# Kernel tuning notes

Measured on AMD Instinct MI355X. Metric: run time of the kernel, lower is better.

## Reference

```python
import jax, jax.numpy as jnp
import numpy as np

HIDDEN = 2048
N_HEADS = 16
HEAD_DIM = HIDDEN // N_HEADS  # 128
KV_DIM = HEAD_DIM             # multi_query: 1 kv head
INTER = 4 * HIDDEN
EPS = 1e-5


def setup_inputs() -> dict:
    key = jax.random.key(0)
    ks = jax.random.split(key, 16)
    s = 0.02
    d = dict(
        hidden_states=jax.random.normal(ks[0], (4, 2048, HIDDEN), jnp.float32),
        ln1_g=jnp.ones((HIDDEN,), jnp.float32),
        ln1_b=jnp.zeros((HIDDEN,), jnp.float32),
        ln2_g=jnp.ones((HIDDEN,), jnp.float32),
        ln2_b=jnp.zeros((HIDDEN,), jnp.float32),
        wq=jax.random.normal(ks[1], (HIDDEN, HIDDEN), jnp.float32) * s,
        bq=jnp.zeros((HIDDEN,), jnp.float32),
        wkv=jax.random.normal(ks[2], (HIDDEN, 2 * KV_DIM), jnp.float32) * s,
        bkv=jnp.zeros((2 * KV_DIM,), jnp.float32),
        wo=jax.random.normal(ks[3], (HIDDEN, HIDDEN), jnp.float32) * s,
        bo=jnp.zeros((HIDDEN,), jnp.float32),
        wfc=jax.random.normal(ks[4], (HIDDEN, INTER), jnp.float32) * s,
        bfc=jnp.zeros((INTER,), jnp.float32),
        wproj=jax.random.normal(ks[5], (INTER, HIDDEN), jnp.float32) * s,
        bproj=jnp.zeros((HIDDEN,), jnp.float32),
    )
    return d


def _ln(x, g, b):
    m = jnp.mean(x, -1, keepdims=True)
    v = jnp.var(x, -1, keepdims=True)
    return (x - m) * jax.lax.rsqrt(v + EPS) * g + b


def _block(x, ln1_g, ln1_b, ln2_g, ln2_b, wq, bq, wkv, bkv, wo, bo, wfc, bfc, wproj, bproj):
    B, S, H = x.shape
    scale = HEAD_DIM ** -0.5
    # --- attention ---
    res = x
    h = _ln(x, ln1_g, ln1_b)
    q = (h @ wq + bq).reshape(B, S, N_HEADS, HEAD_DIM)
    kv = h @ wkv + bkv                       # [B,S,2*KV_DIM]
    k, v = kv[..., :KV_DIM], kv[..., KV_DIM:]  # [B,S,D] single kv head (MQA)
    scores = jnp.einsum('bshd,btd->bhst', q, k) * scale
    causal = jnp.tril(jnp.ones((S, S), bool))
    scores = jnp.where(causal, scores, jnp.finfo(scores.dtype).min)
    probs = jax.nn.softmax(scores, axis=-1)
    attn = jnp.einsum('bhst,btd->bshd', probs, v).reshape(B, S, H)
    x = attn @ wo + bo + res
    # --- mlp ---
    res = x
    h = _ln(x, ln2_g, ln2_b)
    h = jax.nn.gelu(h @ wfc + bfc, approximate=True)  # gelu_pytorch_tanh
    return h @ wproj + bproj + res


def reference(hidden_states, ln1_g, ln1_b, ln2_g, ln2_b, wq, bq, wkv, bkv, wo, bo, wfc, bfc, wproj, bproj):
    return _block(hidden_states, ln1_g, ln1_b, ln2_g, ln2_b, wq, bq, wkv, bkv, wo, bo, wfc, bfc, wproj, bproj)
```

## Files before the change

### kernel.cpp

```cpp
#include <hip/hip_runtime.h>
#include <hip/hip_bf16.h>
#include <math.h>

typedef __bf16 bf16;
typedef __bf16 bf16x8 __attribute__((ext_vector_type(8)));
typedef float  f32x4  __attribute__((ext_vector_type(4)));

#define HID    2048
#define INTER_ 8192
#define SEQ    2048
#define NTOK   8192
#define HD     128

__device__ __forceinline__ f32x4 mfma16(bf16x8 a, bf16x8 b, f32x4 c){
  return __builtin_amdgcn_mfma_f32_16x16x32_bf16(a, b, c, 0, 0, 0);
}

__device__ __forceinline__ void gl_lds16(const void* g, void* l){
  __builtin_amdgcn_global_load_lds((const __attribute__((address_space(1))) void*)g,
                                   (__attribute__((address_space(3))) void*)l,
                                   16, 0, 0);
}

__global__ __launch_bounds__(256)
void convT_k(const float* __restrict__ in, bf16* __restrict__ out, int K, int N)
{
  __shared__ float tile[32][33];
  const int k0 = blockIdx.x * 32, n0 = blockIdx.y * 32;
  const int tx = threadIdx.x & 31, ty = threadIdx.x >> 5;
#pragma unroll
  for (int r = 0; r < 4; r++)
    tile[ty + r*8][tx] = in[(size_t)(k0 + ty + r*8) * N + n0 + tx];
  __syncthreads();
#pragma unroll
  for (int r = 0; r < 4; r++)
    out[(size_t)(n0 + ty + r*8) * K + k0 + tx] = (bf16)tile[tx][ty + r*8];
}

__global__ __launch_bounds__(256)
void ln_k(const float* __restrict__ x, const float* __restrict__ gamma,
          const float* __restrict__ beta, bf16* __restrict__ out)
{
  const int row = blockIdx.x, t = threadIdx.x;
  const float* xr = x + (size_t)row * HID;
  const float4 a = ((const float4*)xr)[t*2];
  const float4 b = ((const float4*)xr)[t*2 + 1];
  float s  = a.x+a.y+a.z+a.w + b.x+b.y+b.z+b.w;
  float ss = a.x*a.x+a.y*a.y+a.z*a.z+a.w*a.w + b.x*b.x+b.y*b.y+b.z*b.z+b.w*b.w;
#pragma unroll
  for (int m = 32; m; m >>= 1){ s += __shfl_xor(s, m); ss += __shfl_xor(ss, m); }
  __shared__ float red[8];
  const int w = t >> 6;
  if ((t & 63) == 0){ red[w*2] = s; red[w*2+1] = ss; }
  __syncthreads();
  s  = red[0] + red[2] + red[4] + red[6];
  ss = red[1] + red[3] + red[5] + red[7];
  const float mean = s * (1.0f/HID);
  const float var  = ss * (1.0f/HID) - mean*mean;
  const float rs   = rsqrtf(var + 1e-5f);
  const int c = t * 8;
  const float xe[8] = {a.x,a.y,a.z,a.w,b.x,b.y,b.z,b.w};
  bf16x8 o;
#pragma unroll
  for (int e = 0; e < 8; e++)
    o[e] = (bf16)((xe[e] - mean) * rs * gamma[c+e] + beta[c+e]);
  *(bf16x8*)(out + (size_t)row*HID + c) = o;
}

template<int EPI>
__global__ __launch_bounds__(256)
void gemm_bt(const bf16* __restrict__ A, const bf16* __restrict__ BT,
             int M, int N, int K,
             const float* __restrict__ bias, const float* __restrict__ bias2,
             const float* __restrict__ res, float* __restrict__ outf,
             bf16* __restrict__ o0, bf16* __restrict__ o1, bf16* __restrict__ o2)
{
  __shared__ bf16 lA[128*32];
  __shared__ bf16 lB[128*32];
  const int t = threadIdx.x, l = t & 63, w = t >> 6;
  int bx = blockIdx.x, by = blockIdx.y;
  {
    const int nwg = gridDim.x * gridDim.y;
    if ((nwg & 7) == 0){
      int wg = by * gridDim.x + bx;
      const int per = nwg >> 3;
      wg = (wg & 7) * per + (wg >> 3);
      bx = wg % gridDim.x; by = wg / gridDim.x;
    }
  }
  const int m0 = bx * 128, n0 = by * 128;
  const int wm = (w >> 1) * 64, wn = (w & 1) * 64;
  const int g16 = l >> 4, c16 = l & 15;
  const f32x4 z4 = {0.f, 0.f, 0.f, 0.f};
  f32x4 acc[4][4];
#pragma unroll
  for (int i = 0; i < 4; i++)
#pragma unroll
    for (int j = 0; j < 4; j++) acc[i][j] = z4;

  const int srow = (t * 16) >> 6;
  const int scol = ((t * 16) & 63) >> 1;

  for (int k0 = 0; k0 < K; k0 += 32){
    __syncthreads();
    gl_lds16(A  + (size_t)(m0 + srow)      * K + k0 + scol, (char*)lA + t*16);
    gl_lds16(A  + (size_t)(m0 + 64 + srow) * K + k0 + scol, (char*)lA + 4096 + t*16);
    gl_lds16(BT + (size_t)(n0 + srow)      * K + k0 + scol, (char*)lB + t*16);
    gl_lds16(BT + (size_t)(n0 + 64 + srow) * K + k0 + scol, (char*)lB + 4096 + t*16);
    __syncthreads();
    bf16x8 af[4], bfv[4];
#pragma unroll
    for (int i = 0; i < 4; i++){
      af[i]  = *(const bf16x8*)&lA[(wm + i*16 + c16)*32 + g16*8];
      bfv[i] = *(const bf16x8*)&lB[(wn + i*16 + c16)*32 + g16*8];
    }
#pragma unroll
    for (int i = 0; i < 4; i++)
#pragma unroll
      for (int j = 0; j < 4; j++)
        acc[i][j] = mfma16(af[i], bfv[j], acc[i][j]);
  }

#pragma unroll
  for (int i = 0; i < 4; i++)
#pragma unroll
    for (int j = 0; j < 4; j++)
#pragma unroll
      for (int r = 0; r < 4; r++){
        const int row = m0 + wm + i*16 + g16*4 + r;
        const int col = n0 + wn + j*16 + c16;
        const float v = acc[i][j][r];
        if constexpr (EPI == 0){
          if (col < HID){
            o0[(size_t)row*HID + col] = (bf16)(v + bias[col]);
          } else {
            const int nn = col - HID;
            const float vv = v + bias2[nn];
            if (nn < HD) o1[(size_t)row*HD + nn] = (bf16)vv;
            else {
              const int d = nn - HD;
              o2[((size_t)(row >> 11)*HD + d)*SEQ + (row & (SEQ-1))] = (bf16)vv;
            }
          }
        } else if constexpr (EPI == 1){
          outf[(size_t)row*HID + col] = v + bias[col] + res[(size_t)row*HID + col];
        } else if constexpr (EPI == 2){
          const float u = v + bias[col];
          const float gg = 0.5f * u * (1.0f + tanhf(0.7978845608028654f * (u + 0.044715f*u*u*u)));
          o0[(size_t)row*INTER_ + col] = (bf16)gg;
        } else {
          float* op = outf + (size_t)row*HID + col;
          *op = v + bias[col] + *op;
        }
      }
}

__global__ __launch_bounds__(256)
void attn_k(const bf16* __restrict__ qbuf, const bf16* __restrict__ kb,
            const bf16* __restrict__ vT, bf16* ob)
{
  __shared__ bf16 pl[4][16][64];
  const int bid0 = blockIdx.x;
  const int bid = ((bid0 & 7) << 7) + (bid0 >> 3);
  const int b  = bid >> 8;
  const int h  = (bid >> 4) & 15;
  const int pr = bid & 15;
  const int t = threadIdx.x, w = t >> 6, l = t & 63;
  const int g16 = l >> 4, c16 = l & 15;
  const float scale = 0.08838834764831845f;
  const f32x4 z4 = {0.f,0.f,0.f,0.f};
  const bf16* kbase = kb + (size_t)b*SEQ*HD;
  const bf16* vbase = vT + (size_t)b*HD*SEQ;

#pragma unroll
  for (int pass = 0; pass < 2; pass++){
    const int qb_i = pass ? (31 - pr) : pr;
    const int q0 = qb_i * 64;
    const bf16* qrow = qbuf + (size_t)(b*SEQ + q0 + w*16 + c16)*HID + h*HD + g16*8;
    bf16x8 qf[4];
#pragma unroll
    for (int dc = 0; dc < 4; dc++) qf[dc] = *(const bf16x8*)(qrow + dc*32);

    f32x4 acc[8];
#pragma unroll
    for (int i = 0; i < 8; i++) acc[i] = z4;
    float mrun[4] = {-1e30f,-1e30f,-1e30f,-1e30f};
    float lrun[4] = {0.f,0.f,0.f,0.f};
    const int qg_ = q0 + w*16 + g16*4;

    for (int kt = 0; kt <= qb_i; kt++){
      const int t0 = kt * 64;
      f32x4 s[4] = {z4, z4, z4, z4};
#pragma unroll
      for (int ks = 0; ks < 4; ks++){
        const bf16* kr = kbase + (size_t)(t0 + ks*16 + c16)*HD + g16*8;
#pragma unroll
        for (int dc = 0; dc < 4; dc++)
          s[ks] = mfma16(qf[dc], *(const bf16x8*)(kr + dc*32), s[ks]);
      }
      const bool last = (kt == qb_i);
      float coef[4];
#pragma unroll
      for (int r = 0; r < 4; r++){
        float sv[4];
#pragma unroll
        for (int ks = 0; ks < 4; ks++) sv[ks] = s[ks][r] * scale;
        if (last){
          const int qg = qg_ + r;
#pragma unroll
          for (int ks = 0; ks < 4; ks++)
            if (t0 + ks*16 + c16 > qg) sv[ks] = -1e30f;
        }
        float mv = fmaxf(fmaxf(sv[0], sv[1]), fmaxf(sv[2], sv[3]));
#pragma unroll
        for (int mk = 1; mk < 16; mk <<= 1) mv = fmaxf(mv, __shfl_xor(mv, mk));
        const float mn = fmaxf(mrun[r], mv);
        float p[4], ps = 0.f;
#pragma unroll
        for (int ks = 0; ks < 4; ks++){ p[ks] = __expf(sv[ks] - mn); ps += p[ks]; }
#pragma unroll
        for (int mk = 1; mk < 16; mk <<= 1) ps += __shfl_xor(ps, mk);
        coef[r] = __expf(mrun[r] - mn);
        lrun[r] = lrun[r]*coef[r] + ps;
        mrun[r] = mn;
#pragma unroll
        for (int ks = 0; ks < 4; ks++)
          pl[w][g16*4 + r][ks*16 + c16] = (bf16)p[ks];
      }
#pragma unroll
      for (int dt = 0; dt < 8; dt++)
#pragma unroll
        for (int r = 0; r < 4; r++) acc[dt][r] *= coef[r];
      const bf16x8 pa0 = *(const bf16x8*)&pl[w][c16][g16*8];
      const bf16x8 pa1 = *(const bf16x8*)&pl[w][c16][32 + g16*8];
#pragma unroll
      for (int dt = 0; dt < 8; dt++){
        const bf16* vr = vbase + (size_t)(dt*16 + c16)*SEQ + t0 + g16*8;
        acc[dt] = mfma16(pa0, *(const bf16x8*)vr,        acc[dt]);
        acc[dt] = mfma16(pa1, *(const bf16x8*)(vr + 32), acc[dt]);
      }
    }
#pragma unroll
    for (int r = 0; r < 4; r++){
      const float inv = 1.0f / lrun[r];
      bf16* orow = ob + (size_t)(b*SEQ + qg_ + r)*HID + h*HD;
#pragma unroll
      for (int dt = 0; dt < 8; dt++)
        orow[dt*16 + c16] = (bf16)(acc[dt][r] * inv);
    }
  }
}

extern "C" void kernel_launch(void* const* d_in, const int* in_sizes, int n_in,
                              void* d_out, int out_size, void* d_ws, size_t ws_size,
                              hipStream_t stream)
{
  const float* x    = (const float*)d_in[0];
  const float* ln1g = (const float*)d_in[1];
  const float* ln1b = (const float*)d_in[2];
  const float* ln2g = (const float*)d_in[3];
  const float* ln2b = (const float*)d_in[4];
  const float* wq   = (const float*)d_in[5];
  const float* bq   = (const float*)d_in[6];
  const float* wkv  = (const float*)d_in[7];
  const float* bkv  = (const float*)d_in[8];
  const float* wo   = (const float*)d_in[9];
  const float* bo   = (const float*)d_in[10];
  const float* wfc  = (const float*)d_in[11];
  const float* bfc  = (const float*)d_in[12];
  const float* wpr  = (const float*)d_in[13];
  const float* bpr  = (const float*)d_in[14];
  float* out = (float*)d_out;
  (void)in_sizes; (void)n_in; (void)out_size;

  char* p = (char*)d_ws;
  auto carve = [&](size_t n){ char* r = p; p += (n + 255) & ~(size_t)255; return r; };
  bf16* wqkvT = (bf16*)carve((size_t)2304*2048*2);
  bf16* woT   = (bf16*)carve((size_t)2048*2048*2);
  bf16* wfcT  = (bf16*)carve((size_t)8192*2048*2);
  bf16* wprT  = (bf16*)carve((size_t)2048*8192*2);
  bf16* hbuf  = (bf16*)carve((size_t)NTOK*2048*2);
  bf16* qbuf  = (bf16*)carve((size_t)NTOK*2048*2);
  bf16* kbuf  = (bf16*)carve((size_t)NTOK*128*2);
  bf16* vbufT = (bf16*)carve((size_t)NTOK*128*2);
  const size_t fixed_bytes = 156237824;
  size_t grows = 2048;
  if (ws_size >= fixed_bytes + (size_t)8192*8192*2)      grows = 8192;
  else if (ws_size >= fixed_bytes + (size_t)4096*8192*2) grows = 4096;
  bf16* gbuf  = (bf16*)carve((size_t)grows*8192*2);

  dim3 B(256);
  convT_k<<<dim3(64, 64),  B, 0, stream>>>(wq,  wqkvT, 2048, 2048);
  convT_k<<<dim3(64, 8),   B, 0, stream>>>(wkv, wqkvT + (size_t)2048*2048, 2048, 256);
  convT_k<<<dim3(64, 64),  B, 0, stream>>>(wo,  woT,  2048, 2048);
  convT_k<<<dim3(64, 256), B, 0, stream>>>(wfc, wfcT, 2048, 8192);
  convT_k<<<dim3(256, 64), B, 0, stream>>>(wpr, wprT, 8192, 2048);

  ln_k<<<NTOK, B, 0, stream>>>(x, ln1g, ln1b, hbuf);
  gemm_bt<0><<<dim3(64, 18), B, 0, stream>>>(hbuf, wqkvT, NTOK, 2304, 2048,
                                             bq, bkv, nullptr, nullptr, qbuf, kbuf, vbufT);
  attn_k<<<1024, B, 0, stream>>>(qbuf, kbuf, vbufT, qbuf );
  gemm_bt<1><<<dim3(64, 16), B, 0, stream>>>(qbuf, woT, NTOK, 2048, 2048,
                                             bo, nullptr, x, out, nullptr, nullptr, nullptr);
  ln_k<<<NTOK, B, 0, stream>>>(out, ln2g, ln2b, hbuf);
  for (size_t c = 0; c < NTOK/grows; c++){
    const size_t ro = c * grows;
    gemm_bt<2><<<dim3(grows/128, 64), B, 0, stream>>>(hbuf + ro*HID, wfcT, (int)grows, 8192, 2048,
                                               bfc, nullptr, nullptr, nullptr, gbuf, nullptr, nullptr);
    gemm_bt<3><<<dim3(grows/128, 16), B, 0, stream>>>(gbuf, wprT, (int)grows, 2048, 8192,
                                               bpr, nullptr, nullptr, out + ro*HID, nullptr, nullptr, nullptr);
  }
}
```

Measured before the change: 1.992 ms.

## Use exp-based tanh in GELU, prefetch V early, alias GELU buffer onto q

Result: faster. 1.948 ms (-2.2%).

```diff
diff --git a/kernel.cpp b/kernel.cpp
--- a/kernel.cpp
+++ b/kernel.cpp
@@ -146,8 +146,9 @@
           outf[(size_t)row*HID + col] = v + bias[col] + res[(size_t)row*HID + col];
         } else if constexpr (EPI == 2){
           const float u = v + bias[col];
-          const float gg = 0.5f * u * (1.0f + tanhf(0.7978845608028654f * (u + 0.044715f*u*u*u)));
-          o0[(size_t)row*INTER_ + col] = (bf16)gg;
+          const float a2 = 1.5957691216057308f * (u + 0.044715f*u*u*u);
+          const float th = 1.0f - 2.0f/(__expf(a2) + 1.0f);
+          o0[(size_t)row*INTER_ + col] = (bf16)(0.5f * u * (1.0f + th));
         } else {
           float* op = outf + (size_t)row*HID + col;
           *op = v + bias[col] + *op;
@@ -198,6 +199,13 @@
         for (int dc = 0; dc < 4; dc++)
           s[ks] = mfma16(qf[dc], *(const bf16x8*)(kr + dc*32), s[ks]);
       }
+      bf16x8 v0a[4], v1a[4];
+#pragma unroll
+      for (int dt = 0; dt < 4; dt++){
+        const bf16* vr = vbase + (size_t)(dt*16 + c16)*SEQ + t0 + g16*8;
+        v0a[dt] = *(const bf16x8*)vr;
+        v1a[dt] = *(const bf16x8*)(vr + 32);
+      }
       const bool last = (kt == qb_i);
       float coef[4];
 #pragma unroll
@@ -234,7 +242,12 @@
       const bf16x8 pa0 = *(const bf16x8*)&pl[w][c16][g16*8];
       const bf16x8 pa1 = *(const bf16x8*)&pl[w][c16][32 + g16*8];
 #pragma unroll
-      for (int dt = 0; dt < 8; dt++){
+      for (int dt = 0; dt < 4; dt++){
+        acc[dt] = mfma16(pa0, v0a[dt], acc[dt]);
+        acc[dt] = mfma16(pa1, v1a[dt], acc[dt]);
+      }
+#pragma unroll
+      for (int dt = 4; dt < 8; dt++){
         const bf16* vr = vbase + (size_t)(dt*16 + c16)*SEQ + t0 + g16*8;
         acc[dt] = mfma16(pa0, *(const bf16x8*)vr,        acc[dt]);
         acc[dt] = mfma16(pa1, *(const bf16x8*)(vr + 32), acc[dt]);
@@ -271,7 +284,7 @@
   const float* wpr  = (const float*)d_in[13];
   const float* bpr  = (const float*)d_in[14];
   float* out = (float*)d_out;
-  (void)in_sizes; (void)n_in; (void)out_size;
+  (void)in_sizes; (void)n_in; (void)out_size; (void)ws_size;
 
   char* p = (char*)d_ws;
   auto carve = [&](size_t n){ char* r = p; p += (n + 255) & ~(size_t)255; return r; };
@@ -283,11 +296,13 @@
   bf16* qbuf  = (bf16*)carve((size_t)NTOK*2048*2);
   bf16* kbuf  = (bf16*)carve((size_t)NTOK*128*2);
   bf16* vbufT = (bf16*)carve((size_t)NTOK*128*2);
-  const size_t fixed_bytes = 156237824;
-  size_t grows = 2048;
-  if (ws_size >= fixed_bytes + (size_t)8192*8192*2)      grows = 8192;
-  else if (ws_size >= fixed_bytes + (size_t)4096*8192*2) grows = 4096;
-  bf16* gbuf  = (bf16*)carve((size_t)grows*8192*2);
+  const size_t grows = 4096;
+  {
+    const size_t span = (size_t)(p - (char*)qbuf);
+    const size_t need = grows * (size_t)INTER_ * 2;
+    if (need > span) carve(need - span);
+  }
+  bf16* gbuf = qbuf;
 
   dim3 B(256);
   convT_k<<<dim3(64, 64),  B, 0, stream>>>(wq,  wqkvT, 2048, 2048);
```
